# Optimization experiments

Hardware: AMD Instinct MI355X
Metric: run time of the kernel (lower is better)

## Reference

```python
import jax, jax.numpy as jnp
import numpy as np
from jax import lax

I_CH = 3
C_CH = 2 * I_CH            # 6
PAIRS = [(i, j) for i in range(C_CH) for j in range(i + 1, C_CH)]  # 15 Givens pairs


def _encoder(x, W, b_enc):
    # CMEncoder stand-in: single SAME 3x3 conv in_channels -> out_channels
    y = lax.conv_general_dilated(x, W, (1, 1), 'SAME',
                                 dimension_numbers=('NCHW', 'OIHW', 'NCHW'))
    return y + b_enc[None, :, None, None]


def _covariance_matrix(s, a):
    # s: [b,C,h,w] per-pixel variances; a: [b,15,h,w] Givens angles
    d = jnp.moveaxis(s, 1, -1)      # [b,h,w,C]
    ang = jnp.moveaxis(a, 1, -1)    # [b,h,w,15]
    b, h, w, Cc = d.shape
    R = jnp.broadcast_to(jnp.eye(Cc, dtype=d.dtype), (b, h, w, Cc, Cc))
    for k, (i, j) in enumerate(PAIRS):
        c = jnp.cos(ang[..., k])[..., None]
        sn = jnp.sin(ang[..., k])[..., None]
        ci = R[..., :, i]
        cj = R[..., :, j]
        R = R.at[..., :, i].set(c * ci + sn * cj)
        R = R.at[..., :, j].set(-sn * ci + c * cj)
    # S = R diag(d) R^T  -> [b,h,w,C,C]
    S = jnp.einsum('bhwmk,bhwk,bhwnk->bhwmn', R, d, R)
    return S, R, d


def reference(x, W, b_enc):
    I = I_CH
    C = C_CH
    p = _encoder(x, W, b_enc)              # [b,30,h,w]
    m = p[:, :C]                           # means [b,6,h,w]
    s = p[:, C:2 * C]
    s = jnp.square(jax.nn.relu(s) - jax.nn.relu(-s))
    s = jnp.clip(s, 1e-6)
    a = 2.0 * jnp.pi * jax.nn.sigmoid(p[:, 2 * C:-I])
    xf = p[:, -I:]                         # [b,3,h,w]
    S, R, d = _covariance_matrix(s, a)
    # S^{-1} = R diag(1/d) R^T (D diagonal, R orthogonal) -> [b,h,w,6,6]
    S_1 = jnp.einsum('bhwmk,bhwk,bhwnk->bhwmn', R, 1.0 / d, R)
    Sxx = S_1[..., :I, :I]
    Syx = S_1[..., I:, :I]
    Q = jnp.matmul(Syx, jnp.linalg.inv(Sxx))   # [b,h,w,3,3]
    mx = m[:, :I]
    my = m[:, I:]
    y = my + jnp.einsum('bijmn,bnij->bmij', Q, xf - mx)
    Sout = jnp.transpose(S, (0, 3, 4, 1, 2))   # [b,6,6,h,w]
    return (xf, m, Sout, y)


def setup_inputs() -> dict:
    key = jax.random.key(0)
    k1, k2, k3 = jax.random.split(key, 3)
    x = jax.random.normal(k1, (4, 3, 256, 256), dtype=jnp.float32)
    W = jax.random.normal(k2, (30, 3, 3, 3), dtype=jnp.float32) * 0.1
    b_enc = jax.random.normal(k3, (30,), dtype=jnp.float32) * 0.1
    return {'x': x, 'W': W, 'b_enc': b_enc}
```

## Files before the change

kernel.cpp:

```cpp
#include <hip/hip_runtime.h>
#include <math.h>

#define HWp 65536

typedef float v2f __attribute__((ext_vector_type(2)));

__device__ __forceinline__ v2f fma2(v2f a, v2f b, v2f c) {
    return __builtin_elementwise_fma(a, b, c);
}
__device__ __forceinline__ void stream_st2(float* p, v2f v) {
    __builtin_nontemporal_store(v, (v2f*)p);
}
__device__ __forceinline__ float vget(v2f v, int px) { return px ? v.y : v.x; }

__global__ __launch_bounds__(128)
void gp_encoder_kernel(const float* __restrict__ x,
                       const float* __restrict__ Wt,
                       const float* __restrict__ be,
                       float* __restrict__ out)
{
    __shared__ v2f Dsh[6][64];
    __shared__ v2f Msh[6][64];
    __shared__ v2f Xsh[3][64];

    const int lane = threadIdx.x & 63;
    const int wid  = threadIdx.x >> 6;

    const int blk  = blockIdx.x;
    const int b    = blk >> 9;
    const int pixb = (blk & 511) << 7;
    const int h    = pixb >> 8;
    const int w0   = pixb & 255;

    const int  c0     = 2 * lane;
    const bool wlo_ok = !(w0 == 0   && lane == 0);
    const bool whi_ok = !(w0 == 128 && lane == 63);
    const int  idx_l  = wlo_ok ? c0 - 1 : c0;
    const int  idx_r  = whi_ok ? c0 + 2 : c0;

    v2f tp[27];
    const float* xb = x + b * 3 * HWp;
    #pragma unroll
    for (int ci = 0; ci < 3; ++ci) {
        #pragma unroll
        for (int kh = 0; kh < 3; ++kh) {
            const int hh = h + kh - 1;
            float lv = 0.f, rv = 0.f;
            v2f   mv = (v2f){0.f, 0.f};
            if ((unsigned)hh < 256u) {
                const float* rp = xb + ci * HWp + hh * 256 + w0;
                mv = *reinterpret_cast<const v2f*>(rp + c0);
                lv = rp[idx_l];
                rv = rp[idx_r];
                lv = wlo_ok ? lv : 0.f;
                rv = whi_ok ? rv : 0.f;
            }
            tp[ci*9 + kh*3 + 0] = (v2f){lv, mv.x};
            tp[ci*9 + kh*3 + 1] = mv;
            tp[ci*9 + kh*3 + 2] = (v2f){mv.y, rv};
        }
    }

    auto conv_ch = [&](int ch) -> v2f {
        const float bb = be[ch];
        v2f acc = (v2f){bb, bb};
        const float* wp = Wt + ch * 27;
        #pragma unroll
        for (int t = 0; t < 27; ++t) {
            const float wt = wp[t];
            acc = fma2(tp[t], (v2f){wt, wt}, acc);
        }
        return acc;
    };

    float* out_xf = out                      + b*3*HWp  + pixb;
    float* out_m  = out + 4*3*HWp            + b*6*HWp  + pixb;
    float* out_S  = out + (4*3+4*6)*HWp      + b*36*HWp + pixb;
    float* out_y  = out + (4*3+4*6+4*36)*HWp + b*3*HWp  + pixb;

    if (wid == 1) {
        v2f pbm[6], pbs[6], pxf[3];
        #pragma unroll
        for (int o = 0; o < 6; ++o) pbm[o] = conv_ch(o);
        #pragma unroll
        for (int o = 0; o < 6; ++o) pbs[o] = conv_ch(6 + o);
        #pragma unroll
        for (int o = 0; o < 3; ++o) pxf[o] = conv_ch(27 + o);

        #pragma unroll
        for (int c = 0; c < 6; ++c) {
            stream_st2(&out_m[c*HWp + c0], pbm[c]);
            Msh[c][lane] = pbm[c];
        }
        #pragma unroll
        for (int i = 0; i < 3; ++i) {
            stream_st2(&out_xf[i*HWp + c0], pxf[i]);
            Xsh[i][lane] = pxf[i];
        }
        #pragma unroll
        for (int k = 0; k < 6; ++k) {
            const v2f s = pbs[k];
            Dsh[k][lane] = __builtin_elementwise_max(s * s, (v2f){1e-6f, 1e-6f});
        }

        __syncthreads();
        return;
    }

    v2f pa[15];
    #pragma unroll
    for (int o = 0; o < 15; ++o)
        pa[o] = conv_ch(12 + o);

    v2f cs[15], ss[15];
    #pragma unroll
    for (int k = 0; k < 15; ++k) {
        const float e0 = __expf(-pa[k].x);
        const float e1 = __expf(-pa[k].y);
        const float g0 = __builtin_amdgcn_rcpf(1.f + e0);
        const float g1 = __builtin_amdgcn_rcpf(1.f + e1);
        cs[k] = (v2f){__builtin_amdgcn_cosf(g0), __builtin_amdgcn_cosf(g1)};
        ss[k] = (v2f){__builtin_amdgcn_sinf(g0), __builtin_amdgcn_sinf(g1)};
    }

    v2f R[6][6];
    #pragma unroll
    for (int r = 0; r < 6; ++r)
        #pragma unroll
        for (int c = 0; c < 6; ++c)
            R[r][c] = (r == c) ? (v2f){1.f, 1.f} : (v2f){0.f, 0.f};

    const int PI_[15] = {0,0,0,0,0,1,1,1,1,2,2,2,3,3,4};
    const int PJ_[15] = {1,2,3,4,5,2,3,4,5,3,4,5,4,5,5};
    #pragma unroll
    for (int k = 0; k < 15; ++k) {
        const int i = PI_[k], j = PJ_[k];
        const v2f c2 = cs[k], s2 = ss[k];
        #pragma unroll
        for (int r = 0; r < 6; ++r) {
            const v2f ri = R[r][i], rj = R[r][j];
            R[r][i] = fma2(c2, ri, s2 * rj);
            R[r][j] = fma2(c2, rj, -(s2 * ri));
        }
    }

    __syncthreads();

    v2f dk[6], mm[6], xx[3];
    #pragma unroll
    for (int k = 0; k < 6; ++k) dk[k] = Dsh[k][lane];
    #pragma unroll
    for (int k = 0; k < 6; ++k) mm[k] = Msh[k][lane];
    #pragma unroll
    for (int k = 0; k < 3; ++k) xx[k] = Xsh[k][lane];

    v2f syx2[3][3], syy2[3][3];
    #pragma unroll
    for (int n = 0; n < 6; ++n) {
        v2f t[6];
        #pragma unroll
        for (int k = 0; k < 6; ++k)
            t[k] = dk[k] * R[n][k];
        #pragma unroll
        for (int r = n; r < 6; ++r) {
            v2f acc = t[0] * R[r][0];
            #pragma unroll
            for (int k = 1; k < 6; ++k)
                acc = fma2(t[k], R[r][k], acc);
            stream_st2(&out_S[(r*6 + n)*HWp + c0], acc);
            if (r != n)
                stream_st2(&out_S[(n*6 + r)*HWp + c0], acc);
            if (r >= 3 && n < 3)  syx2[r-3][n] = acc;
            if (r >= 3 && n >= 3) { syy2[r-3][n-3] = acc;
                                    if (r != n) syy2[n-3][r-3] = acc; }
        }
    }

    float yv[2][3];
    #pragma unroll
    for (int px = 0; px < 2; ++px) {
        const double a00 = (double)vget(syy2[0][0], px), a01 = (double)vget(syy2[0][1], px), a02 = (double)vget(syy2[0][2], px);
        const double a10 = (double)vget(syy2[1][0], px), a11 = (double)vget(syy2[1][1], px), a12 = (double)vget(syy2[1][2], px);
        const double a20 = (double)vget(syy2[2][0], px), a21 = (double)vget(syy2[2][1], px), a22 = (double)vget(syy2[2][2], px);

        const double det = a00*(a11*a22 - a12*a21)
                         - a01*(a10*a22 - a12*a20)
                         + a02*(a10*a21 - a11*a20);
        const double idet = 1.0 / det;

        double inv[3][3];
        inv[0][0] =  (a11*a22 - a12*a21) * idet;
        inv[0][1] = -(a01*a22 - a02*a21) * idet;
        inv[0][2] =  (a01*a12 - a02*a11) * idet;
        inv[1][0] = -(a10*a22 - a12*a20) * idet;
        inv[1][1] =  (a00*a22 - a02*a20) * idet;
        inv[1][2] = -(a00*a12 - a02*a10) * idet;
        inv[2][0] =  (a10*a21 - a11*a20) * idet;
        inv[2][1] = -(a00*a21 - a01*a20) * idet;
        inv[2][2] =  (a00*a11 - a01*a10) * idet;

        double Qp[3][3];
        #pragma unroll
        for (int r = 0; r < 3; ++r)
            #pragma unroll
            for (int c = 0; c < 3; ++c) {
                double acc = 0.0;
                #pragma unroll
                for (int k = 0; k < 3; ++k)
                    acc = fma(inv[r][k], (double)vget(syx2[k][c], px), acc);
                Qp[r][c] = acc;
            }

        #pragma unroll
        for (int i = 0; i < 3; ++i) {
            double acc = (double)vget(mm[3 + i], px);
            #pragma unroll
            for (int n = 0; n < 3; ++n)
                acc = fma(-Qp[i][n], (double)vget(xx[n], px) - (double)vget(mm[n], px), acc);
            yv[px][i] = (float)acc;
        }
    }

    #pragma unroll
    for (int i = 0; i < 3; ++i)
        stream_st2(&out_y[i*HWp + c0], (v2f){yv[0][i], yv[1][i]});
}

extern "C" void kernel_launch(void* const* d_in, const int* in_sizes, int n_in,
                              void* d_out, int out_size, void* d_ws, size_t ws_size,
                              hipStream_t stream) {
    const float* x  = (const float*)d_in[0];
    const float* Wt = (const float*)d_in[1];
    const float* be = (const float*)d_in[2];
    float* out = (float*)d_out;

    dim3 grid(2048);
    dim3 block(128);
    hipLaunchKernelGGL(gp_encoder_kernel, grid, block, 0, stream, x, Wt, be, out);
}
```

Measured before the change: 21.06 us.

## Stage covariance tile in LDS and emit 16-byte stores per full image row

Each block now covers a full 256-pixel row with 256 threads, two angle waves and two conv waves. The 21 unique covariance entries are staged in an LDS tile, then written out as 128-bit nontemporal stores instead of 36 scattered 64-bit stores per thread. The goal is wider, more coalesced writes of the dominant S output. The cost is an extra barrier, about 22KB of LDS that may limit occupancy, and a halved grid.

```diff
diff --git a/kernel.cpp b/kernel.cpp
--- a/kernel.cpp
+++ b/kernel.cpp
@@ -4,6 +4,7 @@
 #define HWp 65536
 
 typedef float v2f __attribute__((ext_vector_type(2)));
+typedef float v4f __attribute__((ext_vector_type(4)));
 
 __device__ __forceinline__ v2f fma2(v2f a, v2f b, v2f c) {
     return __builtin_elementwise_fma(a, b, c);
@@ -11,35 +12,49 @@
 __device__ __forceinline__ void stream_st2(float* p, v2f v) {
     __builtin_nontemporal_store(v, (v2f*)p);
 }
+__device__ __forceinline__ void stream_st4(float* p, v4f v) {
+    __builtin_nontemporal_store(v, (v4f*)p);
+}
 __device__ __forceinline__ float vget(v2f v, int px) { return px ? v.y : v.x; }
 
-__global__ __launch_bounds__(128)
+__host__ __device__ constexpr int TRW(int p) {
+    const int i = p / 6, j = p % 6;
+    const int n = (i < j) ? i : j;
+    const int r = (i < j) ? j : i;
+    return 6*n - (n*(n-1))/2 + (r - n);
+}
+
+__global__ __launch_bounds__(256)
 void gp_encoder_kernel(const float* __restrict__ x,
                        const float* __restrict__ Wt,
                        const float* __restrict__ be,
                        float* __restrict__ out)
 {
-    __shared__ v2f Dsh[6][64];
-    __shared__ v2f Msh[6][64];
-    __shared__ v2f Xsh[3][64];
-
-    const int lane = threadIdx.x & 63;
-    const int wid  = threadIdx.x >> 6;
+    __shared__ v2f Dsh[6][128];
+    __shared__ v2f Msh[6][128];
+    __shared__ v2f Xsh[3][128];
+    __shared__ float Stile[21][260];
+
+    const int tid  = threadIdx.x;
+    const int lane = tid & 63;
+    const int wid  = tid >> 6;
+    const bool isA = wid < 2;
+    const int  half = wid & 1;
 
     const int blk  = blockIdx.x;
-    const int b    = blk >> 9;
-    const int pixb = (blk & 511) << 7;
-    const int h    = pixb >> 8;
-    const int w0   = pixb & 255;
-
-    const int  c0     = 2 * lane;
-    const bool wlo_ok = !(w0 == 0   && lane == 0);
-    const bool whi_ok = !(w0 == 128 && lane == 63);
+    const int b    = blk >> 8;
+    const int h    = blk & 255;
+    const int pixb = h << 8;
+
+    const int  ph = half << 7;
+    const int  c0 = ph + 2 * lane;
+    const bool wlo_ok = (c0 != 0);
+    const bool whi_ok = (c0 != 254);
     const int  idx_l  = wlo_ok ? c0 - 1 : c0;
     const int  idx_r  = whi_ok ? c0 + 2 : c0;
+    const int  xi     = (half << 6) + lane;
 
     v2f tp[27];
-    const float* xb = x + b * 3 * HWp;
     #pragma unroll
     for (int ci = 0; ci < 3; ++ci) {
         #pragma unroll
@@ -48,7 +63,7 @@
             float lv = 0.f, rv = 0.f;
             v2f   mv = (v2f){0.f, 0.f};
             if ((unsigned)hh < 256u) {
-                const float* rp = xb + ci * HWp + hh * 256 + w0;
+                const float* rp = x + (b*3 + ci) * HWp + hh * 256;
                 mv = *reinterpret_cast<const v2f*>(rp + c0);
                 lv = rp[idx_l];
                 rv = rp[idx_r];
@@ -78,7 +93,7 @@
     float* out_S  = out + (4*3+4*6)*HWp      + b*36*HWp + pixb;
     float* out_y  = out + (4*3+4*6+4*36)*HWp + b*3*HWp  + pixb;
 
-    if (wid == 1) {
+    if (!isA) {
         v2f pbm[6], pbs[6], pxf[3];
         #pragma unroll
         for (int o = 0; o < 6; ++o) pbm[o] = conv_ch(o);
@@ -90,19 +105,20 @@
         #pragma unroll
         for (int c = 0; c < 6; ++c) {
             stream_st2(&out_m[c*HWp + c0], pbm[c]);
-            Msh[c][lane] = pbm[c];
+            Msh[c][xi] = pbm[c];
         }
         #pragma unroll
         for (int i = 0; i < 3; ++i) {
             stream_st2(&out_xf[i*HWp + c0], pxf[i]);
-            Xsh[i][lane] = pxf[i];
+            Xsh[i][xi] = pxf[i];
         }
         #pragma unroll
         for (int k = 0; k < 6; ++k) {
             const v2f s = pbs[k];
-            Dsh[k][lane] = __builtin_elementwise_max(s * s, (v2f){1e-6f, 1e-6f});
-        }
-
+            Dsh[k][xi] = __builtin_elementwise_max(s * s, (v2f){1e-6f, 1e-6f});
+        }
+
+        __syncthreads();
         __syncthreads();
         return;
     }
@@ -146,13 +162,9 @@
 
     __syncthreads();
 
-    v2f dk[6], mm[6], xx[3];
-    #pragma unroll
-    for (int k = 0; k < 6; ++k) dk[k] = Dsh[k][lane];
-    #pragma unroll
-    for (int k = 0; k < 6; ++k) mm[k] = Msh[k][lane];
-    #pragma unroll
-    for (int k = 0; k < 3; ++k) xx[k] = Xsh[k][lane];
+    v2f dk[6];
+    #pragma unroll
+    for (int k = 0; k < 6; ++k) dk[k] = Dsh[k][xi];
 
     v2f syx2[3][3], syy2[3][3];
     #pragma unroll
@@ -167,14 +179,33 @@
             #pragma unroll
             for (int k = 1; k < 6; ++k)
                 acc = fma2(t[k], R[r][k], acc);
-            stream_st2(&out_S[(r*6 + n)*HWp + c0], acc);
-            if (r != n)
-                stream_st2(&out_S[(n*6 + r)*HWp + c0], acc);
+            *reinterpret_cast<v2f*>(&Stile[TRW(r*6 + n)][c0]) = acc;
             if (r >= 3 && n < 3)  syx2[r-3][n] = acc;
             if (r >= 3 && n >= 3) { syy2[r-3][n-3] = acc;
                                     if (r != n) syy2[n-3][r-3] = acc; }
         }
     }
+
+    __syncthreads();
+
+    #define STP(p) { v4f v = *reinterpret_cast<const v4f*>(&Stile[TRW(p)][4*lane]); \
+                     stream_st4(&out_S[(p)*HWp + 4*lane], v); }
+    if (half == 0) {
+        STP(0)  STP(2)  STP(4)  STP(6)  STP(8)  STP(10)
+        STP(12) STP(14) STP(16) STP(18) STP(20) STP(22)
+        STP(24) STP(26) STP(28) STP(30) STP(32) STP(34)
+    } else {
+        STP(1)  STP(3)  STP(5)  STP(7)  STP(9)  STP(11)
+        STP(13) STP(15) STP(17) STP(19) STP(21) STP(23)
+        STP(25) STP(27) STP(29) STP(31) STP(33) STP(35)
+    }
+    #undef STP
+
+    v2f mm[6], xx[3];
+    #pragma unroll
+    for (int k = 0; k < 6; ++k) mm[k] = Msh[k][xi];
+    #pragma unroll
+    for (int k = 0; k < 3; ++k) xx[k] = Xsh[k][xi];
 
     float yv[2][3];
     #pragma unroll
@@ -234,7 +265,7 @@
     const float* be = (const float*)d_in[2];
     float* out = (float*)d_out;
 
-    dim3 grid(2048);
-    dim3 block(128);
+    dim3 grid(1024);
+    dim3 block(256);
     hipLaunchKernelGGL(gp_encoder_kernel, grid, block, 0, stream, x, Wt, be, out);
 }
```

Measured after the change: 20.13 us. 1.05x faster.
